# Optimization experiments

Hardware: AMD Instinct MI355X
Metric: run time of the kernel (lower is better)

## Reference

```python
import jax, jax.numpy as jnp
import numpy as np

N = 100000
E = 1600000
F_IN = 256
F_OUT = 128
ALPHA = 0.2  # leaky relu slope


def setup_inputs() -> dict:
    key = jax.random.key(0)
    ks = jax.random.split(key, 8)
    x = jax.random.normal(ks[0], (N, F_IN), dtype=jnp.float32)
    edge_index = jax.random.randint(ks[1], (2, E), 0, N, dtype=jnp.int64)
    edge_attr = jax.random.normal(ks[2], (E,), dtype=jnp.float32)
    # xavier-normal-ish params
    weight = jax.random.normal(ks[3], (F_IN, F_OUT), dtype=jnp.float32) * (1.414 * np.sqrt(2.0 / (F_IN + F_OUT)))
    bias = jnp.zeros((F_OUT,), dtype=jnp.float32)
    a_l = jax.random.normal(ks[4], (F_OUT,), dtype=jnp.float32) * 0.1
    a_r = jax.random.normal(ks[5], (F_OUT,), dtype=jnp.float32) * 0.1
    fc = jax.random.normal(ks[6], (F_OUT, 1), dtype=jnp.float32) * (1.414 * np.sqrt(2.0 / (F_OUT + 1)))
    bf = jnp.zeros((1,), dtype=jnp.float32)
    return {"x": x, "edge_index": edge_index, "edge_attr": edge_attr,
            "weight": weight, "bias": bias, "a_l": a_l, "a_r": a_r,
            "fc": fc, "bf": bf}


def _segment_softmax(val, seg, num_segments):
    # numerically stable softmax over edges grouped by destination row
    seg_max = jax.ops.segment_max(val, seg, num_segments=num_segments)
    val = jnp.exp(val - seg_max[seg])
    seg_sum = jax.ops.segment_sum(val, seg, num_segments=num_segments)
    return val / (seg_sum[seg] + 1e-16)


def reference(x, edge_index, edge_attr, weight, bias, a_l, a_r, fc, bf):
    # dropout layers are identity in eval mode (deterministic reference)
    h = x @ weight                                   # [N, F_OUT]
    row, col = edge_index[0], edge_index[1]          # dst, src
    # GAT-style edge attention: leaky_relu(a_l.h[dst] + a_r.h[src])
    score_l = h @ a_l                                # [N]
    score_r = h @ a_r                                # [N]
    e = score_l[row] + score_r[col]                  # [E]
    e = jnp.where(e > 0, e, ALPHA * e)
    # row-softmax normalization over incoming edges of each dst node
    val = _segment_softmax(e, row, N)                # [E]
    # spmm: out[i] = sum_{(i,j) in E} val_ij * h[j]
    val_h = jax.ops.segment_sum(val[:, None] * h[col], row, num_segments=N)  # [N, F_OUT]
    val_h = jnp.where(jnp.isnan(val_h), 0.0, val_h)
    val_h = val_h + bias
    # NodeAdaptiveEncoder: relu(x) + sigmoid(x@fc + bf) * min(x, 0)
    gate = jax.nn.sigmoid(val_h @ fc + bf)           # [N, 1]
    out = jnp.where(val_h < 0, 0.0, val_h) + gate * jnp.where(val_h > 0, 0.0, val_h)
    return out
```

## Files before the change

kernel.cpp:

```cpp
#include <hip/hip_runtime.h>

#define N_NODES 100000
#define N_EDGES 1600000
#define FIN 256
#define FOUT 128
#define LRELU_ALPHA 0.2f

#define NBUCKET 391
#define PBLOCKS 256
#define PCHUNK  (N_EDGES / PBLOCKS)
#define BCAP    5120

using bf16x8 = __attribute__((ext_vector_type(8))) short;
using f32x4  = __attribute__((ext_vector_type(4))) float;
using v2f    = __attribute__((ext_vector_type(2))) float;

static __device__ __forceinline__ unsigned short f2bf(float f) {
    union { float f; unsigned u; } v; v.f = f;
    unsigned r = (v.u + 0x7FFF + ((v.u >> 16) & 1)) >> 16;
    return (unsigned short)r;
}

static __device__ __forceinline__ bf16x8 cvt8(float4 a, float4 b) {
    union { bf16x8 v; unsigned short u[8]; } r;
    r.u[0] = f2bf(a.x); r.u[1] = f2bf(a.y); r.u[2] = f2bf(a.z); r.u[3] = f2bf(a.w);
    r.u[4] = f2bf(b.x); r.u[5] = f2bf(b.y); r.u[6] = f2bf(b.z); r.u[7] = f2bf(b.w);
    return r.v;
}

static __device__ __forceinline__ void gld_lds16(const unsigned short* g, unsigned short* l) {
    __builtin_amdgcn_global_load_lds(
        (const __attribute__((address_space(1))) unsigned int*)g,
        (__attribute__((address_space(3))) unsigned int*)l, 16, 0, 0);
}

static __device__ __forceinline__ v2f up2(unsigned u) {
    v2f r;
    r.x = __int_as_float((int)(u << 16));
    r.y = __int_as_float((int)(u & 0xFFFF0000u));
    return r;
}

__global__ void k_wt(const float* __restrict__ w, unsigned short* __restrict__ wt_sw,
                     int* __restrict__ bcnt)
{
    if (blockIdx.x == 0)
        for (int z = threadIdx.x; z < NBUCKET; z += 256) bcnt[z] = 0;
    int i = blockIdx.x * blockDim.x + threadIdx.x;
    if (i >= FIN * FOUT) return;
    int k = i >> 7, n = i & 127;
    wt_sw[n * FIN + (((k >> 3) ^ (n & 7)) << 3) + (k & 7)] = f2bf(w[k * FOUT + n]);
}

__global__ __launch_bounds__(256, 2) void k_gemm3(
    const float* __restrict__ x, const unsigned short* __restrict__ wt_sw,
    const float* __restrict__ a_l, const float* __restrict__ a_r,
    unsigned short* __restrict__ hb, float* __restrict__ score_l,
    float* __restrict__ score_r)
{
    __shared__ unsigned short wlds[FOUT * FIN];

    const int tid  = threadIdx.x;
    const int lane = tid & 63;
    const int wid  = tid >> 6;
    const int m    = lane & 15;
    const int q    = lane >> 4;

    {
        const unsigned short* g = wt_sw + wid * 8192;
        unsigned short*       l = wlds  + wid * 8192;
#pragma unroll
        for (int i = 0; i < 16; ++i)
            gld_lds16(g + i * 512 + lane * 8, l + i * 512);
    }

    const int row0 = blockIdx.x * 128 + wid * 32;
    int r0 = row0 + m;       if (r0 > N_NODES - 1) r0 = N_NODES - 1;
    int r1 = row0 + 16 + m;  if (r1 > N_NODES - 1) r1 = N_NODES - 1;
    const float* xp0 = x + (long)r0 * FIN + q * 8;
    const float* xp1 = x + (long)r1 * FIN + q * 8;

    float4 xb[2][2][2];
    xb[0][0][0] = *(const float4*)(xp0);        xb[0][0][1] = *(const float4*)(xp0 + 4);
    xb[0][1][0] = *(const float4*)(xp1);        xb[0][1][1] = *(const float4*)(xp1 + 4);
    xb[1][0][0] = *(const float4*)(xp0 + 32);   xb[1][0][1] = *(const float4*)(xp0 + 36);
    xb[1][1][0] = *(const float4*)(xp1 + 32);   xb[1][1][1] = *(const float4*)(xp1 + 36);

    f32x4 acc[2][8];
#pragma unroll
    for (int mt = 0; mt < 2; ++mt)
#pragma unroll
        for (int nt = 0; nt < 8; ++nt) acc[mt][nt] = (f32x4){0.f, 0.f, 0.f, 0.f};

    __syncthreads();

    const int xr = m & 7;

    bf16x8 bfr[2][8];
#pragma unroll
    for (int nt = 0; nt < 8; ++nt)
        bfr[0][nt] = *(const bf16x8*)&wlds[(nt * 16 + m) * FIN + ((q ^ xr) << 3)];

#pragma unroll
    for (int s = 0; s < 8; ++s) {
        const int p = s & 1;
        bf16x8 a0 = cvt8(xb[p][0][0], xb[p][0][1]);
        bf16x8 a1 = cvt8(xb[p][1][0], xb[p][1][1]);
        if (s + 2 < 8) {
            xb[p][0][0] = *(const float4*)(xp0 + (s + 2) * 32);
            xb[p][0][1] = *(const float4*)(xp0 + (s + 2) * 32 + 4);
            xb[p][1][0] = *(const float4*)(xp1 + (s + 2) * 32);
            xb[p][1][1] = *(const float4*)(xp1 + (s + 2) * 32 + 4);
        }
        if (s + 1 < 8) {
#pragma unroll
            for (int nt = 0; nt < 8; ++nt)
                bfr[1 - p][nt] = *(const bf16x8*)
                    &wlds[(nt * 16 + m) * FIN + ((((s + 1) * 4 + q) ^ xr) << 3)];
        }
#pragma unroll
        for (int nt = 0; nt < 8; ++nt) {
            acc[0][nt] = __builtin_amdgcn_mfma_f32_16x16x32_bf16(a0, bfr[p][nt], acc[0][nt], 0, 0, 0);
            acc[1][nt] = __builtin_amdgcn_mfma_f32_16x16x32_bf16(a1, bfr[p][nt], acc[1][nt], 0, 0, 0);
        }
    }

    float al[8], ar[8];
#pragma unroll
    for (int nt = 0; nt < 8; ++nt) { al[nt] = a_l[nt * 16 + m]; ar[nt] = a_r[nt * 16 + m]; }

#pragma unroll
    for (int mt = 0; mt < 2; ++mt) {
#pragma unroll
        for (int r = 0; r < 4; ++r) {
            const int node = row0 + mt * 16 + q * 4 + r;
            const bool ok = node < N_NODES;
            float sl = 0.f, sr = 0.f;
#pragma unroll
            for (int nt = 0; nt < 8; ++nt) {
                float v = acc[mt][nt][r];
                if (ok) hb[node * FOUT + nt * 16 + m] = f2bf(v);
                sl = fmaf(v, al[nt], sl);
                sr = fmaf(v, ar[nt], sr);
            }
#pragma unroll
            for (int msk = 1; msk < 16; msk <<= 1) {
                sl += __shfl_xor(sl, msk, 64);
                sr += __shfl_xor(sr, msk, 64);
            }
            if (ok && m == 0) { score_l[node] = sl; score_r[node] = sr; }
        }
    }
}

__global__ __launch_bounds__(512) void k_part(const int* __restrict__ ei,
                                              int* __restrict__ bcnt,
                                              unsigned* __restrict__ part)
{
    __shared__ unsigned staging[PCHUNK];
    __shared__ unsigned short bkt[PCHUNK];
    __shared__ int cnt[512];
    __shared__ int loc[512];
    __shared__ int gbase[NBUCKET];

    const int tid = threadIdx.x;
    const int e0  = blockIdx.x * PCHUNK;

    cnt[tid] = 0;
    __syncthreads();

    for (int i = tid; i < PCHUNK; i += 512)
        atomicAdd(&cnt[ei[e0 + i] >> 8], 1);
    __syncthreads();

    int v = cnt[tid];
    loc[tid] = v;
    __syncthreads();
    for (int off = 1; off < 512; off <<= 1) {
        int t = (tid >= off) ? loc[tid - off] : 0;
        __syncthreads();
        loc[tid] += t;
        __syncthreads();
    }
    int excl = loc[tid] - v;
    if (tid < NBUCKET && v > 0) gbase[tid] = atomicAdd(&bcnt[tid], v);
    loc[tid] = excl;
    cnt[tid] = excl;
    __syncthreads();

    for (int i = tid; i < PCHUNK; i += 512) {
        int dst = ei[e0 + i];
        int src = ei[N_EDGES + e0 + i];
        int b = dst >> 8;
        unsigned rec = ((unsigned)(dst & 255) << 17) | (unsigned)src;
        int p = atomicAdd(&cnt[b], 1);
        staging[p] = rec;
        bkt[p] = (unsigned short)b;
    }
    __syncthreads();

    for (int i = tid; i < PCHUNK; i += 512) {
        int b = bkt[i];
        int off = gbase[b] + (i - loc[b]);
        if (off < BCAP) part[b * BCAP + off] = staging[i];
    }
}

__global__ __launch_bounds__(512) void k_bucket(const unsigned* __restrict__ part,
                                                const int* __restrict__ bcnt,
                                                int* __restrict__ rowbeg,
                                                int* __restrict__ rowend,
                                                unsigned* __restrict__ csrs)
{
    __shared__ unsigned rin[BCAP];
    __shared__ unsigned rs[BCAP];
    __shared__ int hist[256];
    __shared__ int tmp[512];

    const int b   = blockIdx.x;
    const int tid = threadIdx.x;
    const int beg = b * BCAP;
    int cnt = bcnt[b];
    if (cnt > BCAP) cnt = BCAP;
    const int d0 = b << 8;

    if (tid < 256) hist[tid] = 0;
    __syncthreads();

    for (int i = tid; i < cnt; i += 512) {
        unsigned rec = part[beg + i];
        rin[i] = rec;
        atomicAdd(&hist[rec >> 17], 1);
    }
    __syncthreads();

    int v = (tid < 256) ? hist[tid] : 0;
    tmp[tid] = v;
    __syncthreads();
    for (int off = 1; off < 512; off <<= 1) {
        int t = (tid >= off) ? tmp[tid - off] : 0;
        __syncthreads();
        tmp[tid] += t;
        __syncthreads();
    }
    if (tid < 256) {
        int excl = tmp[tid] - v;
        hist[tid] = excl;
        int d = d0 + tid;
        if (d < N_NODES) { rowbeg[d] = beg + excl; rowend[d] = beg + excl + v; }
    }
    __syncthreads();

    for (int i = tid; i < cnt; i += 512) {
        unsigned rec = rin[i];
        int p = atomicAdd(&hist[rec >> 17], 1);
        rs[p] = rec;
    }
    __syncthreads();

    for (int i = tid; i < cnt; i += 512)
        csrs[beg + i] = rs[i];
}

__global__ __launch_bounds__(256) void k_spmm_gate(
    const int* __restrict__ rowbeg, const int* __restrict__ rowend,
    const unsigned* __restrict__ csrs,
    const unsigned short* __restrict__ hb,
    const float* __restrict__ score_l, const float* __restrict__ score_r,
    const float* __restrict__ bias, const float* __restrict__ fc,
    const float* __restrict__ bf, float* __restrict__ out)
{
    const int lane = threadIdx.x & 63;
    const int g    = lane >> 4;
    const int t    = lane & 15;
    const int node = blockIdx.x * 4 + (threadIdx.x >> 6);
    if (node >= N_NODES) return;

    const int beg = rowbeg[node], end = rowend[node];
    const int deg = end - beg;
    const float sl = score_l[node];

    v2f a0 = {0.f, 0.f}, a1 = {0.f, 0.f}, a2 = {0.f, 0.f}, a3 = {0.f, 0.f};
    float denom = 0.f;

    if (deg > 0) {
        const int nit  = (deg + 3) >> 2;
        const int last = end - 1;

        int j = beg + g;
        int jc = j <= last ? j : last;
        unsigned recA = csrs[jc];
        unsigned recB = recA;
        if (nit > 1) {
            int j1 = j + 4;
            int jc1 = j1 <= last ? j1 : last;
            recB = csrs[jc1];
        }
        int   sA   = recA & 0x1FFFF;
        float srA  = score_r[sA];
        uint4 rowA = *(const uint4*)&hb[sA * FOUT + t * 8];
        bool  vA   = j < end;

        for (int i = 0; i < nit; ++i) {
            unsigned recC = recB;
            if (i + 2 < nit) {
                int j2 = j + 8;
                int jc2 = j2 <= last ? j2 : last;
                recC = csrs[jc2];
            }
            float srB = 0.f;
            uint4 rowB = {0u, 0u, 0u, 0u};
            bool  vB = false;
            if (i + 1 < nit) {
                int sB = recB & 0x1FFFF;
                srB  = score_r[sB];
                rowB = *(const uint4*)&hb[sB * FOUT + t * 8];
                vB   = (j + 4) < end;
            }
            float e = sl + srA;
            e = e > 0.f ? e : LRELU_ALPHA * e;
            float w = vA ? __expf(e) : 0.f;
            denom += w;
            v2f w2 = {w, w};
            a0 += w2 * up2(rowA.x);  a1 += w2 * up2(rowA.y);
            a2 += w2 * up2(rowA.z);  a3 += w2 * up2(rowA.w);
            recB = recC; srA = srB; rowA = rowB; vA = vB;
            j += 4;
        }
    }

    float accf[8] = {a0.x, a0.y, a1.x, a1.y, a2.x, a2.y, a3.x, a3.y};
#pragma unroll
    for (int k = 0; k < 8; ++k) {
        accf[k] += __shfl_xor(accf[k], 16, 64);
        accf[k] += __shfl_xor(accf[k], 32, 64);
    }
    denom += __shfl_xor(denom, 16, 64);
    denom += __shfl_xor(denom, 32, 64);

    const float inv = 1.0f / (denom + 1e-16f);

    float vx[8];
    float gp = 0.f;
#pragma unroll
    for (int i = 0; i < 8; ++i) {
        vx[i] = fmaf(accf[i], inv, bias[t * 8 + i]);
        gp = fmaf(vx[i], fc[t * 8 + i], gp);
    }
#pragma unroll
    for (int msk = 1; msk < 16; msk <<= 1) gp += __shfl_xor(gp, msk, 64);
    const float gate = 1.0f / (1.0f + __expf(-(gp + bf[0])));

    float4 o;
    float* ov = &o.x;
    if (g == 0) {
#pragma unroll
        for (int i = 0; i < 4; ++i) {
            float v2 = vx[i];
            ov[i] = (v2 < 0.f ? 0.f : v2) + gate * (v2 > 0.f ? 0.f : v2);
        }
        *(float4*)&out[node * FOUT + t * 8] = o;
    } else if (g == 1) {
#pragma unroll
        for (int i = 0; i < 4; ++i) {
            float v2 = vx[4 + i];
            ov[i] = (v2 < 0.f ? 0.f : v2) + gate * (v2 > 0.f ? 0.f : v2);
        }
        *(float4*)&out[node * FOUT + t * 8 + 4] = o;
    }
}

extern "C" void kernel_launch(void* const* d_in, const int* in_sizes, int n_in,
                              void* d_out, int out_size, void* d_ws, size_t ws_size,
                              hipStream_t stream)
{
    const float* x      = (const float*)d_in[0];
    const int*   ei     = (const int*)d_in[1];
    const float* weight = (const float*)d_in[3];
    const float* bias   = (const float*)d_in[4];
    const float* a_l    = (const float*)d_in[5];
    const float* a_r    = (const float*)d_in[6];
    const float* fc     = (const float*)d_in[7];
    const float* bf     = (const float*)d_in[8];
    float* out = (float*)d_out;

    char* ws = (char*)d_ws;
    unsigned short* hb      = (unsigned short*)(ws);
    unsigned short* wt_sw   = (unsigned short*)(ws + 25600000);
    float*          score_l = (float*)(ws + 25665536);
    float*          score_r = (float*)(ws + 26065536);
    int*            bcnt    = (int*)  (ws + 26465536);
    int*            rowbeg  = (int*)  (ws + 26467584);
    int*            rowend  = (int*)  (ws + 26867584);
    unsigned*       part    = (unsigned*)(ws + 27267584);
    unsigned*       csrs    = (unsigned*)(ws + 35275264);

    k_wt<<<(FIN * FOUT + 255) / 256, 256, 0, stream>>>(weight, wt_sw, bcnt);

    k_gemm3<<<(N_NODES + 127) / 128, 256, 0, stream>>>(
        x, wt_sw, a_l, a_r, hb, score_l, score_r);

    k_part<<<PBLOCKS, 512, 0, stream>>>(ei, bcnt, part);
    k_bucket<<<NBUCKET, 512, 0, stream>>>(part, bcnt, rowbeg, rowend, csrs);

    k_spmm_gate<<<(N_NODES + 3) / 4, 256, 0, stream>>>(
        rowbeg, rowend, csrs, hb, score_l, score_r, bias, fc, bf, out);
}
```

Before: 294.8 us.

## Store features as fp16 and unroll the SpMM gather loop by two

The GEMM epilogue now stores the projected features in fp16 instead of bf16, and the SpMM reads them back with half-to-float conversions. The SpMM gather loop is restructured into a 2x-unrolled software pipeline with branchless leaky-relu and an explicit tail, so there are fewer conditional moves per edge. fp16 has more mantissa bits but a smaller range, so large values could overflow. The hardware conversion may be cheaper than the shift-based bf16 unpack.

```diff
diff --git a/kernel.cpp b/kernel.cpp
--- a/kernel.cpp
+++ b/kernel.cpp
@@ -13,7 +13,6 @@
 
 using bf16x8 = __attribute__((ext_vector_type(8))) short;
 using f32x4  = __attribute__((ext_vector_type(4))) float;
-using v2f    = __attribute__((ext_vector_type(2))) float;
 
 static __device__ __forceinline__ unsigned short f2bf(float f) {
     union { float f; unsigned u; } v; v.f = f;
@@ -34,11 +33,16 @@
         (__attribute__((address_space(3))) unsigned int*)l, 16, 0, 0);
 }
 
-static __device__ __forceinline__ v2f up2(unsigned u) {
-    v2f r;
-    r.x = __int_as_float((int)(u << 16));
-    r.y = __int_as_float((int)(u & 0xFFFF0000u));
-    return r;
+static __device__ __forceinline__ void acc8(float* acc, uint4 r, float w) {
+    union { uint4 u; _Float16 h[8]; } c; c.u = r;
+#pragma unroll
+    for (int k = 0; k < 8; ++k)
+        acc[k] = fmaf((float)c.h[k], w, acc[k]);
+}
+
+static __device__ __forceinline__ float edgew(float sl, float sr) {
+    float e = sl + sr;
+    return __expf(fmaf(fminf(e, 0.f), LRELU_ALPHA, fmaxf(e, 0.f)));
 }
 
 __global__ void k_wt(const float* __restrict__ w, unsigned short* __restrict__ wt_sw,
@@ -129,6 +133,8 @@
 #pragma unroll
     for (int nt = 0; nt < 8; ++nt) { al[nt] = a_l[nt * 16 + m]; ar[nt] = a_r[nt * 16 + m]; }
 
+    _Float16* hh = (_Float16*)hb;
+
 #pragma unroll
     for (int mt = 0; mt < 2; ++mt) {
 #pragma unroll
@@ -139,7 +145,7 @@
 #pragma unroll
             for (int nt = 0; nt < 8; ++nt) {
                 float v = acc[mt][nt][r];
-                if (ok) hb[node * FOUT + nt * 16 + m] = f2bf(v);
+                if (ok) hh[node * FOUT + nt * 16 + m] = (_Float16)v;
                 sl = fmaf(v, al[nt], sl);
                 sr = fmaf(v, ar[nt], sr);
             }
@@ -277,63 +283,69 @@
     if (node >= N_NODES) return;
 
     const int beg = rowbeg[node], end = rowend[node];
-    const int deg = end - beg;
     const float sl = score_l[node];
-
-    v2f a0 = {0.f, 0.f}, a1 = {0.f, 0.f}, a2 = {0.f, 0.f}, a3 = {0.f, 0.f};
+    const unsigned short* __restrict__ hq = hb + (t << 3);
+
+    float acc[8] = {0.f, 0.f, 0.f, 0.f, 0.f, 0.f, 0.f, 0.f};
     float denom = 0.f;
 
-    if (deg > 0) {
-        const int nit  = (deg + 3) >> 2;
+    if (end > beg) {
+        const int nit  = (end - beg + 3) >> 2;
+        const int nv   = nit - 1;
         const int last = end - 1;
-
         int j = beg + g;
-        int jc = j <= last ? j : last;
-        unsigned recA = csrs[jc];
-        unsigned recB = recA;
-        if (nit > 1) {
-            int j1 = j + 4;
-            int jc1 = j1 <= last ? j1 : last;
-            recB = csrs[jc1];
-        }
-        int   sA   = recA & 0x1FFFF;
-        float srA  = score_r[sA];
-        uint4 rowA = *(const uint4*)&hb[sA * FOUT + t * 8];
-        bool  vA   = j < end;
-
-        for (int i = 0; i < nit; ++i) {
-            unsigned recC = recB;
-            if (i + 2 < nit) {
-                int j2 = j + 8;
-                int jc2 = j2 <= last ? j2 : last;
-                recC = csrs[jc2];
-            }
-            float srB = 0.f;
-            uint4 rowB = {0u, 0u, 0u, 0u};
-            bool  vB = false;
-            if (i + 1 < nit) {
-                int sB = recB & 0x1FFFF;
-                srB  = score_r[sB];
-                rowB = *(const uint4*)&hb[sB * FOUT + t * 8];
-                vB   = (j + 4) < end;
-            }
-            float e = sl + srA;
-            e = e > 0.f ? e : LRELU_ALPHA * e;
-            float w = vA ? __expf(e) : 0.f;
+
+        unsigned rec1;
+        float sr0; uint4 r0;
+        {
+            unsigned rec0 = csrs[min(j, last)];
+            rec1 = csrs[min(j + 4, last)];
+            int s0 = rec0 & 0x1FFFF;
+            sr0 = score_r[s0];
+            r0  = *(const uint4*)(hq + (s0 << 7));
+        }
+
+        int i = 0;
+        for (; i + 2 <= nv; i += 2) {
+            unsigned rec2 = csrs[min(j + 8, last)];
+            int s1 = rec1 & 0x1FFFF;
+            float sr1 = score_r[s1];
+            uint4 r1  = *(const uint4*)(hq + (s1 << 7));
+            float w0 = edgew(sl, sr0);
+            denom += w0;
+            acc8(acc, r0, w0);
+            j += 4;
+            unsigned rec3 = csrs[min(j + 8, last)];
+            int s2 = rec2 & 0x1FFFF;
+            float sr2 = score_r[s2];
+            uint4 r2  = *(const uint4*)(hq + (s2 << 7));
+            float w1 = edgew(sl, sr1);
+            denom += w1;
+            acc8(acc, r1, w1);
+            j += 4;
+            rec1 = rec3; sr0 = sr2; r0 = r2;
+        }
+        if (i < nv) {
+            int s1 = rec1 & 0x1FFFF;
+            float sr1 = score_r[s1];
+            uint4 r1  = *(const uint4*)(hq + (s1 << 7));
+            float w0 = edgew(sl, sr0);
+            denom += w0;
+            acc8(acc, r0, w0);
+            j += 4;
+            sr0 = sr1; r0 = r1;
+        }
+        {
+            float w = (j < end) ? edgew(sl, sr0) : 0.f;
             denom += w;
-            v2f w2 = {w, w};
-            a0 += w2 * up2(rowA.x);  a1 += w2 * up2(rowA.y);
-            a2 += w2 * up2(rowA.z);  a3 += w2 * up2(rowA.w);
-            recB = recC; srA = srB; rowA = rowB; vA = vB;
-            j += 4;
-        }
-    }
-
-    float accf[8] = {a0.x, a0.y, a1.x, a1.y, a2.x, a2.y, a3.x, a3.y};
+            acc8(acc, r0, w);
+        }
+    }
+
 #pragma unroll
     for (int k = 0; k < 8; ++k) {
-        accf[k] += __shfl_xor(accf[k], 16, 64);
-        accf[k] += __shfl_xor(accf[k], 32, 64);
+        acc[k] += __shfl_xor(acc[k], 16, 64);
+        acc[k] += __shfl_xor(acc[k], 32, 64);
     }
     denom += __shfl_xor(denom, 16, 64);
     denom += __shfl_xor(denom, 32, 64);
@@ -344,7 +356,7 @@
     float gp = 0.f;
 #pragma unroll
     for (int i = 0; i < 8; ++i) {
-        vx[i] = fmaf(accf[i], inv, bias[t * 8 + i]);
+        vx[i] = fmaf(acc[i], inv, bias[t * 8 + i]);
         gp = fmaf(vx[i], fc[t * 8 + i], gp);
     }
 #pragma unroll
```

Result: no change. 293.0 us (-0.6%).
